# Kernel optimization log

Measured on AMD Instinct MI355X. Metric: run time of the kernel, lower is better.

Reference implementation:

```python
import jax, jax.numpy as jnp
import numpy as np

N = 100000      # nodes
E = 1600000     # edges
IN = 128        # in_channels
HEADS = 4
HID = 32        # hidden_channels (per-head dim)
HD = HEADS * HID  # 128, concat output dim
OUT = 2         # out_channels


def setup_inputs() -> dict:
    key = jax.random.key(0)
    ks = jax.random.split(key, 18)

    def lin(kw, kb, fan_in, fan_out):
        lim = 1.0 / np.sqrt(fan_in)
        W = jax.random.uniform(kw, (fan_in, fan_out), jnp.float32, -lim, lim)
        b = jax.random.uniform(kb, (fan_out,), jnp.float32, -lim, lim)
        return W, b

    x = jax.random.normal(ks[0], (N, IN), jnp.float32)
    edge_index = jax.random.randint(ks[1], (2, E), 0, N, jnp.int32)

    Wq, bq = lin(ks[2], ks[3], IN, HD)   # lin_query
    Wk, bk = lin(ks[4], ks[5], IN, HD)   # lin_key
    Wv, bv = lin(ks[6], ks[7], IN, HD)   # lin_value
    Ws, bs = lin(ks[8], ks[9], IN, HD)   # lin_skip (root weight)
    W1, b1 = lin(ks[10], ks[11], HD, 6 * HEADS)  # readout Linear(128, 24)
    W2, b2 = lin(ks[12], ks[13], 6 * HEADS, 8)   # readout Linear(24, 8)
    W3, b3 = lin(ks[14], ks[15], 8, OUT)         # readout Linear(8, 2)

    return {"x": x, "edge_index": edge_index,
            "Wq": Wq, "bq": bq, "Wk": Wk, "bk": bk, "Wv": Wv, "bv": bv,
            "Ws": Ws, "bs": bs, "W1": W1, "b1": b1, "W2": W2, "b2": b2,
            "W3": W3, "b3": b3}


def _tanhshrink(z):
    return z - jnp.tanh(z)


def reference(x, edge_index, Wq, bq, Wk, bk, Wv, bv, Ws, bs,
              W1, b1, W2, b2, W3, b3):
    n = x.shape[0]
    src, dst = edge_index[0], edge_index[1]  # messages flow src -> dst

    # TransformerConv: per-node Q/K/V projections, reshaped to heads
    q = (x @ Wq + bq).reshape(n, HEADS, HID)
    k = (x @ Wk + bk).reshape(n, HEADS, HID)
    v = (x @ Wv + bv).reshape(n, HEADS, HID)

    # per-edge gather + attention logits [E, H]
    scale = 1.0 / np.float32(np.sqrt(HID))
    scores = jnp.einsum('ehd,ehd->eh', q[dst], k[src]) * scale

    # segment softmax over incoming edges of each dst node (numerically stable)
    m = jax.ops.segment_max(scores, dst, num_segments=n)
    m = jnp.where(jnp.isfinite(m), m, 0.0)  # guard isolated nodes
    e = jnp.exp(scores - m[dst])
    denom = jax.ops.segment_sum(e, dst, num_segments=n)
    alpha = e / denom[dst]  # [E, H]

    # weighted scatter-aggregate of values, concat heads, add root skip
    agg = jax.ops.segment_sum(alpha[:, :, None] * v[src], dst,
                              num_segments=n).reshape(n, HD)
    h = jnp.tanh(agg + x @ Ws + bs)  # bn() in source is an identity reshape

    # readout MLP (Dropout p=0.01 omitted: eval mode)
    h1 = _tanhshrink(h @ W1 + b1)
    h2 = _tanhshrink(h1 @ W2 + b2)
    return h2 @ W3 + b3
```

## Files before the change

### kernel.cpp

```cpp
#include <hip/hip_runtime.h>
#include <hip/hip_bf16.h>
#include <hip/hip_fp16.h>
#include <math.h>

#define NN 100000
#define EE 1600000
#define HD_ 128
#define PART 8
#define RNG 12500
#define PBLK 128
#define SCATB (PART * PBLK)
#define PSTRIDE (PBLK * 256)
#define CAP 64
#define PROJ_GRID 512
#define NTILES (NN / 16)

typedef float f32x4 __attribute__((ext_vector_type(4)));
typedef _Float16 f16x8 __attribute__((ext_vector_type(8)));
typedef _Float16 f16x2 __attribute__((ext_vector_type(2)));
typedef float accf4 __attribute__((ext_vector_type(4)));

__device__ __forceinline__ float fast_tanh(float z) {
    float az = fabsf(z);
    float e = __expf(-2.f * az);
    float t = (1.f - e) / (1.f + e);
    return copysignf(t, z);
}

struct alignas(16) h8 { __half2 h[4]; };
struct alignas(8)  h4 { __half2 a, b; };

__global__ __launch_bounds__(256) void wt_kernel(
    const float* __restrict__ Wq, const float* __restrict__ Wk,
    const float* __restrict__ Wv, const float* __restrict__ Ws,
    __half* __restrict__ Wt)
{
    const int t = blockIdx.x * 256 + threadIdx.x;
    const int lane = t & 63;
    const int kt = (t >> 6) & 3;
    const int ct = (t >> 8) & 7;
    const int mat = t >> 11;
    const float* Wm = (mat == 0) ? Wq : (mat == 1) ? Wk : (mat == 2) ? Wv : Ws;
    const int col = ct * 16 + (lane & 15);
    const int k0 = kt * 32 + (lane >> 4) * 8;
    h8 hh;
#pragma unroll
    for (int j = 0; j < 4; ++j) {
        hh.h[j] = __floats2half2_rn(Wm[(size_t)(k0 + 2 * j) * 128 + col],
                                    Wm[(size_t)(k0 + 2 * j + 1) * 128 + col]);
    }
    *reinterpret_cast<h8*>(Wt + (size_t)t * 8) = hh;
}

__global__ __launch_bounds__(256) void proj_mfma(
    const float* __restrict__ x, const __half* __restrict__ Wt,
    const float* __restrict__ bq, const float* __restrict__ bk,
    const float* __restrict__ bv, const float* __restrict__ bs,
    __half* __restrict__ Qh, __half* __restrict__ Sh, __half* __restrict__ KV)
{
    __shared__ __half xs[16][136];
    __shared__ __half ys[16][520];
    const int tid = threadIdx.x;
    const int w = tid >> 6;
    const int lane = tid & 63;

    f16x8 wf[32];
    {
        const __half* wbase = Wt + (size_t)w * 16384;
#pragma unroll
        for (int i = 0; i < 32; ++i)
            wf[i] = *reinterpret_cast<const f16x8*>(
                wbase + (size_t)(i * 64 + lane) * 8);
    }

    const float* bm = (w == 0) ? bq : (w == 1) ? bk : (w == 2) ? bv : bs;
    const float sc = (w == 0) ? 0.17677669529663687f : 1.f;

    const int srow = tid & 15;
    const int sk0 = (tid >> 4) * 8;

    int t = blockIdx.x;
    f32x4 ra, rb;
    if (t < NTILES) {
        const f32x4* xp = reinterpret_cast<const f32x4*>(
            x + (size_t)(t * 16 + srow) * 128 + sk0);
        ra = __builtin_nontemporal_load(xp);
        rb = __builtin_nontemporal_load(xp + 1);
    }

    for (; t < NTILES; t += PROJ_GRID) {
        const int n0 = t * 16;

        {
            h8 hh;
            hh.h[0] = __floats2half2_rn(ra.x, ra.y);
            hh.h[1] = __floats2half2_rn(ra.z, ra.w);
            hh.h[2] = __floats2half2_rn(rb.x, rb.y);
            hh.h[3] = __floats2half2_rn(rb.z, rb.w);
            *reinterpret_cast<h8*>(&xs[srow][sk0]) = hh;
        }
        __syncthreads();

        if (t + PROJ_GRID < NTILES) {
            const f32x4* xp = reinterpret_cast<const f32x4*>(
                x + (size_t)((t + PROJ_GRID) * 16 + srow) * 128 + sk0);
            ra = __builtin_nontemporal_load(xp);
            rb = __builtin_nontemporal_load(xp + 1);
        }

        f16x8 bx[4];
#pragma unroll
        for (int kt = 0; kt < 4; ++kt)
            bx[kt] = *reinterpret_cast<const f16x8*>(
                &xs[lane & 15][kt * 32 + (lane >> 4) * 8]);

#pragma unroll
        for (int ct = 0; ct < 8; ++ct) {
            accf4 acc = {0.f, 0.f, 0.f, 0.f};
#pragma unroll
            for (int kt = 0; kt < 4; ++kt)
                acc = __builtin_amdgcn_mfma_f32_16x16x32_f16(
                    wf[ct * 4 + kt], bx[kt], acc, 0, 0, 0);
            const float4 bb = *reinterpret_cast<const float4*>(
                bm + ct * 16 + ((lane >> 4) << 2));
            h4 o;
            o.a = __floats2half2_rn((acc[0] + bb.x) * sc, (acc[1] + bb.y) * sc);
            o.b = __floats2half2_rn((acc[2] + bb.z) * sc, (acc[3] + bb.w) * sc);
            *reinterpret_cast<h4*>(
                &ys[lane & 15][w * 128 + ct * 16 + ((lane >> 4) << 2)]) = o;
        }
        __syncthreads();

        {
            const int node = tid >> 4;
            const int c8 = (tid & 15) * 8;
            h8 q = *reinterpret_cast<h8*>(&ys[node][c8]);
            h8 k = *reinterpret_cast<h8*>(&ys[node][128 + c8]);
            h8 v = *reinterpret_cast<h8*>(&ys[node][256 + c8]);
            h8 s = *reinterpret_cast<h8*>(&ys[node][384 + c8]);
            *reinterpret_cast<h8*>(Qh + (size_t)(n0 + node) * 128 + c8) = q;
            *reinterpret_cast<h8*>(KV + (size_t)(n0 + node) * 256 + c8) = k;
            *reinterpret_cast<h8*>(KV + (size_t)(n0 + node) * 256 + 128 + c8) = v;
            *reinterpret_cast<h8*>(Sh + (size_t)(n0 + node) * 128 + c8) = s;
        }
        __syncthreads();
    }
}

__global__ __launch_bounds__(256) void bucket_scatter(
    const int* __restrict__ ei, int* __restrict__ cnt, int* __restrict__ ssrc)
{
    const int g = blockIdx.x & (PART - 1);
    const int bg = blockIdx.x >> 3;
    const int lo = g * RNG;
    const int hi = lo + RNG;
    for (int e = bg * 256 + threadIdx.x; e < EE; e += PSTRIDE) {
        const int d = ei[EE + e];
        if (d >= lo && d < hi) {
            int pos = atomicAdd(&cnt[d], 1);
            if (pos < CAP) ssrc[(d << 6) | pos] = ei[e];
        }
    }
}

__global__ __launch_bounds__(256) void attn_kernel(
    const __half* __restrict__ Qh, const __half* __restrict__ KV,
    const __half* __restrict__ Sh,
    const int* __restrict__ cnt, const int* __restrict__ ssrc,
    __half* __restrict__ hbuf)
{
    const int wid = threadIdx.x >> 6;
    const int lane = threadIdx.x & 63;
    const int node = blockIdx.x * 4 + wid;
    const int eg = lane >> 4;
    const int li = lane & 15;

    h8 qq = *reinterpret_cast<const h8*>(Qh + (size_t)node * 128 + li * 8);
    f16x2 qp[4];
#pragma unroll
    for (int j = 0; j < 4; ++j)
        qp[j] = *reinterpret_cast<const f16x2*>(&qq.h[j]);

    float a[8];
#pragma unroll
    for (int j = 0; j < 8; ++j) a[j] = 0.f;
    float l = 0.f;

    const int st = node << 6;
    int dg = cnt[node];
    if (dg > CAP) dg = CAP;

    for (int it = 0; it < dg; it += 16) {
        const __half* rows[4];
        bool val[4];
#pragma unroll
        for (int b = 0; b < 4; ++b) {
            const int e = it + b * 4 + eg;
            val[b] = e < dg;
            const int src = ssrc[st + (val[b] ? e : 0)];
            rows[b] = KV + (size_t)src * 256 + li * 8;
        }

        h8 kk[4], vv[4];
#pragma unroll
        for (int b = 0; b < 4; ++b) {
            kk[b] = *reinterpret_cast<const h8*>(rows[b]);
            vv[b] = *reinterpret_cast<const h8*>(rows[b] + 128);
        }

        float p[4];
#pragma unroll
        for (int b = 0; b < 4; ++b) {
            float s = 0.f;
#if __has_builtin(__builtin_amdgcn_fdot2)
#pragma unroll
            for (int j = 0; j < 4; ++j)
                s = __builtin_amdgcn_fdot2(
                        qp[j], *reinterpret_cast<const f16x2*>(&kk[b].h[j]),
                        s, false);
#else
#pragma unroll
            for (int j = 0; j < 4; ++j) {
                const float2 kf = __half22float2(kk[b].h[j]);
                const float2 qf = __half22float2(qq.h[j]);
                s = fmaf(qf.x, kf.x, s);
                s = fmaf(qf.y, kf.y, s);
            }
#endif
            p[b] = s;
        }

#pragma unroll
        for (int b = 0; b < 4; ++b) {
            p[b] += __shfl_xor(p[b], 1);
            p[b] += __shfl_xor(p[b], 2);
        }

        float w[4];
#pragma unroll
        for (int b = 0; b < 4; ++b) {
            w[b] = val[b] ? __expf(p[b]) : 0.f;
            l += w[b];
        }

#pragma unroll
        for (int b = 0; b < 4; ++b) {
#pragma unroll
            for (int j = 0; j < 4; ++j) {
                const float2 vf = __half22float2(vv[b].h[j]);
                a[2 * j]     = fmaf(w[b], vf.x, a[2 * j]);
                a[2 * j + 1] = fmaf(w[b], vf.y, a[2 * j + 1]);
            }
        }
    }

#pragma unroll
    for (int j = 0; j < 8; ++j) {
        a[j] += __shfl_xor(a[j], 16);
        a[j] += __shfl_xor(a[j], 32);
    }
    l += __shfl_xor(l, 16);
    l += __shfl_xor(l, 32);

    const float inv = (l > 0.f) ? 1.f / l : 0.f;

    if (eg == 0) {
        const h8 ss = *reinterpret_cast<const h8*>(Sh + (size_t)node * 128 + li * 8);
        h8 ho;
#pragma unroll
        for (int j = 0; j < 4; ++j) {
            const float2 sf = __half22float2(ss.h[j]);
            const float h0 = fast_tanh(a[2 * j] * inv + sf.x);
            const float h1 = fast_tanh(a[2 * j + 1] * inv + sf.y);
            ho.h[j] = __floats2half2_rn(h0, h1);
        }
        *reinterpret_cast<h8*>(hbuf + (size_t)node * 128 + li * 8) = ho;
    }
}

__global__ __launch_bounds__(256) void mlp_kernel(
    const __half* __restrict__ hbuf,
    const float* __restrict__ W1, const float* __restrict__ b1,
    const float* __restrict__ W2, const float* __restrict__ b2,
    const float* __restrict__ W3, const float* __restrict__ b3,
    float* __restrict__ out)
{
    __shared__ float W1s[128][24];
    __shared__ float W2s[24][8];
    __shared__ float W3s[8][2];
    __shared__ float b1s[24], b2s[8], b3s[2];

    const int tid = threadIdx.x;

    {
        const float4* src = reinterpret_cast<const float4*>(W1 + tid * 12);
        float4* dst = reinterpret_cast<float4*>(&W1s[0][0] + tid * 12);
        dst[0] = src[0];
        dst[1] = src[1];
        dst[2] = src[2];
        if (tid < 48)
            reinterpret_cast<float4*>(&W2s[0][0])[tid] =
                reinterpret_cast<const float4*>(W2)[tid];
        if (tid < 4)
            reinterpret_cast<float4*>(&W3s[0][0])[tid] =
                reinterpret_cast<const float4*>(W3)[tid];
        if (tid < 24) b1s[tid] = b1[tid];
        if (tid < 8)  b2s[tid] = b2[tid];
        if (tid < 2)  b3s[tid] = b3[tid];
    }
    __syncthreads();

    const int node = blockIdx.x * 256 + tid;
    if (node >= NN) return;

    float t24[24];
#pragma unroll
    for (int j = 0; j < 24; ++j) t24[j] = b1s[j];

    const h8* hrow = reinterpret_cast<const h8*>(hbuf + (size_t)node * 128);
#pragma unroll
    for (int c = 0; c < 16; ++c) {
        const h8 hh = hrow[c];
        float hf[8];
#pragma unroll
        for (int j = 0; j < 4; ++j) {
            const float2 f = __half22float2(hh.h[j]);
            hf[2 * j] = f.x;
            hf[2 * j + 1] = f.y;
        }
#pragma unroll
        for (int i = 0; i < 8; ++i) {
            const int kk = c * 8 + i;
#pragma unroll
            for (int j4 = 0; j4 < 6; ++j4) {
                const float4 w4 = *reinterpret_cast<const float4*>(&W1s[kk][j4 * 4]);
                t24[j4 * 4 + 0] = fmaf(hf[i], w4.x, t24[j4 * 4 + 0]);
                t24[j4 * 4 + 1] = fmaf(hf[i], w4.y, t24[j4 * 4 + 1]);
                t24[j4 * 4 + 2] = fmaf(hf[i], w4.z, t24[j4 * 4 + 2]);
                t24[j4 * 4 + 3] = fmaf(hf[i], w4.w, t24[j4 * 4 + 3]);
            }
        }
    }

    float u8[8];
#pragma unroll
    for (int j = 0; j < 8; ++j) u8[j] = b2s[j];
#pragma unroll
    for (int kk = 0; kk < 24; ++kk) {
        const float hv = t24[kk] - fast_tanh(t24[kk]);
#pragma unroll
        for (int j = 0; j < 8; ++j) u8[j] = fmaf(hv, W2s[kk][j], u8[j]);
    }

    float o0 = b3s[0], o1 = b3s[1];
#pragma unroll
    for (int kk = 0; kk < 8; ++kk) {
        const float hv = u8[kk] - fast_tanh(u8[kk]);
        o0 = fmaf(hv, W3s[kk][0], o0);
        o1 = fmaf(hv, W3s[kk][1], o1);
    }
    *reinterpret_cast<float2*>(out + (size_t)node * 2) = make_float2(o0, o1);
}

extern "C" void kernel_launch(void* const* d_in, const int* in_sizes, int n_in,
                              void* d_out, int out_size, void* d_ws, size_t ws_size,
                              hipStream_t stream)
{
    const float* x  = (const float*)d_in[0];
    const int*   ei = (const int*)d_in[1];
    const float* Wq = (const float*)d_in[2];
    const float* bq = (const float*)d_in[3];
    const float* Wk = (const float*)d_in[4];
    const float* bk = (const float*)d_in[5];
    const float* Wv = (const float*)d_in[6];
    const float* bv = (const float*)d_in[7];
    const float* Ws = (const float*)d_in[8];
    const float* bs = (const float*)d_in[9];
    const float* W1 = (const float*)d_in[10];
    const float* b1 = (const float*)d_in[11];
    const float* W2 = (const float*)d_in[12];
    const float* b2 = (const float*)d_in[13];
    const float* W3 = (const float*)d_in[14];
    const float* b3 = (const float*)d_in[15];
    float* out = (float*)d_out;

    __half* ws = (__half*)d_ws;
    __half* Qh = ws;
    __half* Sh = Qh + (size_t)NN * HD_;
    __half* KV = Sh + (size_t)NN * HD_;
    __half* hbuf = KV + (size_t)NN * 256;
    __half* Wt = hbuf + (size_t)NN * HD_;
    int* cnt  = (int*)(Wt + 65536);
    int* ssrc = cnt + NN;

    (void)hipMemsetAsync(cnt, 0, NN * sizeof(int), stream);

    wt_kernel<<<32, 256, 0, stream>>>(Wq, Wk, Wv, Ws, Wt);
    bucket_scatter<<<SCATB, 256, 0, stream>>>(ei, cnt, ssrc);
    proj_mfma<<<PROJ_GRID, 256, 0, stream>>>(x, Wt, bq, bk, bv, bs, Qh, Sh, KV);
    attn_kernel<<<NN / 4, 256, 0, stream>>>(Qh, KV, Sh, cnt, ssrc, hbuf);
    mlp_kernel<<<(NN + 255) / 256, 256, 0, stream>>>(hbuf, W1, b1, W2, b2,
                                                     W3, b3, out);
}
```

Measured before the change: 254.5 us.

## Split projection weights across 512-thread blocks with 32-node tiles

```diff
diff --git a/kernel.cpp b/kernel.cpp
--- a/kernel.cpp
+++ b/kernel.cpp
@@ -13,7 +13,7 @@
 #define PSTRIDE (PBLK * 256)
 #define CAP 64
 #define PROJ_GRID 512
-#define NTILES (NN / 16)
+#define NT32 (NN / 32)
 
 typedef float f32x4 __attribute__((ext_vector_type(4)));
 typedef _Float16 f16x8 __attribute__((ext_vector_type(8)));
@@ -52,44 +52,59 @@
     *reinterpret_cast<h8*>(Wt + (size_t)t * 8) = hh;
 }
 
-__global__ __launch_bounds__(256) void proj_mfma(
+__global__ __launch_bounds__(256) void bucket_scatter(
+    const int* __restrict__ ei, int* __restrict__ cnt, int* __restrict__ ssrc)
+{
+    const int g = blockIdx.x & (PART - 1);
+    const int bg = blockIdx.x >> 3;
+    const int lo = g * RNG;
+    const int hi = lo + RNG;
+    for (int e = bg * 256 + threadIdx.x; e < EE; e += PSTRIDE) {
+        const int d = ei[EE + e];
+        if (d >= lo && d < hi) {
+            int pos = atomicAdd(&cnt[d], 1);
+            if (pos < CAP) ssrc[(d << 6) | pos] = ei[e];
+        }
+    }
+}
+
+__global__ __launch_bounds__(512, 4) void proj_mfma(
     const float* __restrict__ x, const __half* __restrict__ Wt,
     const float* __restrict__ bq, const float* __restrict__ bk,
     const float* __restrict__ bv, const float* __restrict__ bs,
     __half* __restrict__ Qh, __half* __restrict__ Sh, __half* __restrict__ KV)
 {
-    __shared__ __half xs[16][136];
-    __shared__ __half ys[16][520];
+    __shared__ __half xs[32][136];
+    __shared__ __half ys[32][520];
     const int tid = threadIdx.x;
-    const int w = tid >> 6;
+    const int wid = tid >> 6;
     const int lane = tid & 63;
-
-    f16x8 wf[32];
-    {
-        const __half* wbase = Wt + (size_t)w * 16384;
-#pragma unroll
-        for (int i = 0; i < 32; ++i)
-            wf[i] = *reinterpret_cast<const f16x8*>(
-                wbase + (size_t)(i * 64 + lane) * 8);
-    }
+    const int w = wid & 3;
+    const int ch = wid >> 2;
+
+    f16x8 wf[16];
+#pragma unroll
+    for (int i = 0; i < 16; ++i)
+        wf[i] = *reinterpret_cast<const f16x8*>(
+            Wt + (size_t)(((w * 32 + ch * 16 + i) * 64) + lane) * 8);
 
     const float* bm = (w == 0) ? bq : (w == 1) ? bk : (w == 2) ? bv : bs;
     const float sc = (w == 0) ? 0.17677669529663687f : 1.f;
 
-    const int srow = tid & 15;
-    const int sk0 = (tid >> 4) * 8;
+    const int srow = tid & 31;
+    const int sk0 = (tid >> 5) * 8;
 
     int t = blockIdx.x;
     f32x4 ra, rb;
-    if (t < NTILES) {
+    if (t < NT32) {
         const f32x4* xp = reinterpret_cast<const f32x4*>(
-            x + (size_t)(t * 16 + srow) * 128 + sk0);
+            x + (size_t)(t * 32 + srow) * 128 + sk0);
         ra = __builtin_nontemporal_load(xp);
         rb = __builtin_nontemporal_load(xp + 1);
     }
 
-    for (; t < NTILES; t += PROJ_GRID) {
-        const int n0 = t * 16;
+    for (; t < NT32; t += PROJ_GRID) {
+        const int n0 = t * 32;
 
         {
             h8 hh;
@@ -101,33 +116,40 @@
         }
         __syncthreads();
 
-        if (t + PROJ_GRID < NTILES) {
+        if (t + PROJ_GRID < NT32) {
             const f32x4* xp = reinterpret_cast<const f32x4*>(
-                x + (size_t)((t + PROJ_GRID) * 16 + srow) * 128 + sk0);
+                x + (size_t)((t + PROJ_GRID) * 32 + srow) * 128 + sk0);
             ra = __builtin_nontemporal_load(xp);
             rb = __builtin_nontemporal_load(xp + 1);
         }
 
-        f16x8 bx[4];
-#pragma unroll
-        for (int kt = 0; kt < 4; ++kt)
-            bx[kt] = *reinterpret_cast<const f16x8*>(
-                &xs[lane & 15][kt * 32 + (lane >> 4) * 8]);
-
-#pragma unroll
-        for (int ct = 0; ct < 8; ++ct) {
-            accf4 acc = {0.f, 0.f, 0.f, 0.f};
+#pragma unroll
+        for (int nh = 0; nh < 2; ++nh) {
+            f16x8 bx[4];
 #pragma unroll
             for (int kt = 0; kt < 4; ++kt)
-                acc = __builtin_amdgcn_mfma_f32_16x16x32_f16(
-                    wf[ct * 4 + kt], bx[kt], acc, 0, 0, 0);
-            const float4 bb = *reinterpret_cast<const float4*>(
-                bm + ct * 16 + ((lane >> 4) << 2));
-            h4 o;
-            o.a = __floats2half2_rn((acc[0] + bb.x) * sc, (acc[1] + bb.y) * sc);
-            o.b = __floats2half2_rn((acc[2] + bb.z) * sc, (acc[3] + bb.w) * sc);
-            *reinterpret_cast<h4*>(
-                &ys[lane & 15][w * 128 + ct * 16 + ((lane >> 4) << 2)]) = o;
+                bx[kt] = *reinterpret_cast<const f16x8*>(
+                    &xs[nh * 16 + (lane & 15)][kt * 32 + (lane >> 4) * 8]);
+
+#pragma unroll
+            for (int c4 = 0; c4 < 4; ++c4) {
+                accf4 acc = {0.f, 0.f, 0.f, 0.f};
+#pragma unroll
+                for (int kt = 0; kt < 4; ++kt)
+                    acc = __builtin_amdgcn_mfma_f32_16x16x32_f16(
+                        wf[c4 * 4 + kt], bx[kt], acc, 0, 0, 0);
+                const int ct = ch * 4 + c4;
+                const float4 bb = *reinterpret_cast<const float4*>(
+                    bm + ct * 16 + ((lane >> 4) << 2));
+                h4 o;
+                o.a = __floats2half2_rn((acc[0] + bb.x) * sc,
+                                        (acc[1] + bb.y) * sc);
+                o.b = __floats2half2_rn((acc[2] + bb.z) * sc,
+                                        (acc[3] + bb.w) * sc);
+                *reinterpret_cast<h4*>(
+                    &ys[nh * 16 + (lane & 15)]
+                       [w * 128 + ct * 16 + ((lane >> 4) << 2)]) = o;
+            }
         }
         __syncthreads();
 
@@ -142,23 +164,6 @@
             *reinterpret_cast<h8*>(KV + (size_t)(n0 + node) * 256 + c8) = k;
             *reinterpret_cast<h8*>(KV + (size_t)(n0 + node) * 256 + 128 + c8) = v;
             *reinterpret_cast<h8*>(Sh + (size_t)(n0 + node) * 128 + c8) = s;
-        }
-        __syncthreads();
-    }
-}
-
-__global__ __launch_bounds__(256) void bucket_scatter(
-    const int* __restrict__ ei, int* __restrict__ cnt, int* __restrict__ ssrc)
-{
-    const int g = blockIdx.x & (PART - 1);
-    const int bg = blockIdx.x >> 3;
-    const int lo = g * RNG;
-    const int hi = lo + RNG;
-    for (int e = bg * 256 + threadIdx.x; e < EE; e += PSTRIDE) {
-        const int d = ei[EE + e];
-        if (d >= lo && d < hi) {
-            int pos = atomicAdd(&cnt[d], 1);
-            if (pos < CAP) ssrc[(d << 6) | pos] = ei[e];
         }
     }
 }
@@ -397,7 +402,7 @@
 
     wt_kernel<<<32, 256, 0, stream>>>(Wq, Wk, Wv, Ws, Wt);
     bucket_scatter<<<SCATB, 256, 0, stream>>>(ei, cnt, ssrc);
-    proj_mfma<<<PROJ_GRID, 256, 0, stream>>>(x, Wt, bq, bk, bv, bs, Qh, Sh, KV);
+    proj_mfma<<<PROJ_GRID, 512, 0, stream>>>(x, Wt, bq, bk, bv, bs, Qh, Sh, KV);
     attn_kernel<<<NN / 4, 256, 0, stream>>>(Qh, KV, Sh, cnt, ssrc, hbuf);
     mlp_kernel<<<(NN + 255) / 256, 256, 0, stream>>>(hbuf, W1, b1, W2, b2,
                                                      W3, b3, out);
```

Measured after the change: 264.3 us. 3.9% more time.
